# Kernel optimization log

Measured on AMD Instinct MI355X. Metric: run time of the kernel, lower is better.

The kernel has to match this reference:

```python
import jax, jax.numpy as jnp
import numpy as np

DEPTH = 7  # complete binary trees with 2**DEPTH = 128 leaves

B, L = 4096, 128
V, E, OUT = 100000, 128, 3


def setup_inputs() -> dict:
    key = jax.random.key(0)
    ks = jax.random.split(key, 6)
    tokens = jax.random.randint(ks[0], (B, L), 0, V, dtype=jnp.int64)
    embedding = jax.random.normal(ks[1], (V, E), dtype=jnp.float32)
    # tree_layer: Linear(2E -> E); torch stores weight as [out, in]
    W_tree = jax.random.normal(ks[2], (E, 2 * E), dtype=jnp.float32) * (1.0 / np.sqrt(2 * E))
    b_tree = jax.random.normal(ks[3], (E,), dtype=jnp.float32) * 0.01
    # classifier_layer: Linear(E -> OUT)
    W_cls = jax.random.normal(ks[4], (OUT, E), dtype=jnp.float32) * (1.0 / np.sqrt(E))
    b_cls = jax.random.normal(ks[5], (OUT,), dtype=jnp.float32) * 0.01
    return {"tokens": tokens, "embedding": embedding, "W_tree": W_tree,
            "b_tree": b_tree, "W_cls": W_cls, "b_cls": b_cls}


def reference(tokens, embedding, W_tree, b_tree, W_cls, b_cls):
    # Leaf embeddings: gather rows of the embedding table. [B, L, E]
    reps = embedding[tokens]
    # Level-synchronous bottom-up composition (depth-batched across all trees):
    # at each level, pair adjacent nodes, concat features, apply tree_layer + tanh.
    for _ in range(DEPTH):
        left = reps[:, 0::2, :]   # [B, n/2, E]
        right = reps[:, 1::2, :]  # [B, n/2, E]
        combined = jnp.concatenate([left, right], axis=-1)  # [B, n/2, 2E]
        reps = jnp.tanh(jnp.einsum('bnh,eh->bne', combined, W_tree) + b_tree)
    roots = reps[:, 0, :]  # [B, E]
    return roots @ W_cls.T + b_cls  # [B, OUT]
```

## Files before the change

### kernel.cpp

```cpp
#include <hip/hip_runtime.h>
#include <hip/hip_fp16.h>


typedef _Float16 half8 __attribute__((ext_vector_type(8)));
typedef float floatx4 __attribute__((ext_vector_type(4)));

#define STRIDE 264
#define UROW   33
#define NPAIR  2048

__device__ __forceinline__ float fast_tanh(float x) {
  float e = __expf(2.f * x);
  return 1.f - 2.f * __builtin_amdgcn_rcpf(e + 1.f);
}

__device__ __forceinline__ unsigned pkrtz(float a, float b) {
  auto h = __builtin_amdgcn_cvt_pkrtz(a, b);
  return __builtin_bit_cast(unsigned, h);
}

__device__ __forceinline__ void gather_leafhalf(int tok, const float* __restrict__ emb,
                                                _Float16* buf, int row, int seg) {
  const float4* src = (const float4*)emb + (size_t)tok * 32 + (seg & 1) * 16;
  uint4* dst = (uint4*)buf + row * UROW + seg * 8;
#pragma unroll
  for (int j = 0; j < 8; ++j) {
    float4 x = src[2 * j], y = src[2 * j + 1];
    uint4 w;
    w.x = pkrtz(x.x, x.y); w.y = pkrtz(x.z, x.w);
    w.z = pkrtz(y.x, y.y); w.w = pkrtz(y.z, y.w);
    dst[j] = w;
  }
}

__device__ __forceinline__ void mfma_k256(const _Float16* arow, const half8 (&Wf)[2][8],
                                          floatx4 (&accO)[2]) {
  floatx4 aA[2], aB[2];
  aA[0] = (floatx4){0.f, 0.f, 0.f, 0.f}; aA[1] = (floatx4){0.f, 0.f, 0.f, 0.f};
  aB[0] = (floatx4){0.f, 0.f, 0.f, 0.f}; aB[1] = (floatx4){0.f, 0.f, 0.f, 0.f};
#pragma unroll
  for (int ks = 0; ks < 4; ++ks) {
    half8 x0 = *(const half8*)(arow + ks * 32);
    half8 x1 = *(const half8*)(arow + (ks + 4) * 32);
    aA[0] = __builtin_amdgcn_mfma_f32_16x16x32_f16(x0, Wf[0][ks],     aA[0], 0, 0, 0);
    aB[0] = __builtin_amdgcn_mfma_f32_16x16x32_f16(x1, Wf[0][ks + 4], aB[0], 0, 0, 0);
    aA[1] = __builtin_amdgcn_mfma_f32_16x16x32_f16(x0, Wf[1][ks],     aA[1], 0, 0, 0);
    aB[1] = __builtin_amdgcn_mfma_f32_16x16x32_f16(x1, Wf[1][ks + 4], aB[1], 0, 0, 0);
  }
  accO[0] = aA[0] + aB[0];
  accO[1] = aA[1] + aB[1];
}

template<int MT, int MOUT>
__device__ __forceinline__ void level_std(
    const _Float16* inb, _Float16* outb,
    const half8 (&Wf)[2][8], const float (&bias)[2],
    int nbase, int l15, int quad)
{
  floatx4 acc[MT][2];
  if (MT == 1) {
    floatx4 a2[2];
    mfma_k256(inb + l15 * STRIDE + quad * 8, Wf, a2);
    acc[0][0] = a2[0]; acc[0][1] = a2[1];
  } else {
#pragma unroll
    for (int m = 0; m < MT; ++m) {
      acc[m][0] = (floatx4){0.f, 0.f, 0.f, 0.f};
      acc[m][1] = (floatx4){0.f, 0.f, 0.f, 0.f};
    }
#pragma unroll
    for (int m = 0; m < MT; ++m) {
      const _Float16* arow = inb + (m * 16 + l15) * STRIDE + quad * 8;
#pragma unroll
      for (int ks = 0; ks < 8; ++ks) {
        half8 a = *(const half8*)(arow + ks * 32);
        acc[m][0] = __builtin_amdgcn_mfma_f32_16x16x32_f16(a, Wf[0][ks], acc[m][0], 0, 0, 0);
        acc[m][1] = __builtin_amdgcn_mfma_f32_16x16x32_f16(a, Wf[1][ks], acc[m][1], 0, 0, 0);
      }
    }
  }

  const int mrow = quad * 4;
#pragma unroll
  for (int m = 0; m < MT; ++m)
#pragma unroll
    for (int i = 0; i < 2; ++i) {
      const int col = (nbase + i) * 16 + l15;
#pragma unroll
      for (int r = 0; r < 4; ++r) {
        const int node = m * 16 + mrow + r;
        if (node < MOUT) {
          float v = fast_tanh(acc[m][i][r] + bias[i]);
          outb[(node >> 1) * STRIDE + (node & 1) * 128 + col] = (_Float16)v;
        }
      }
    }
}

__global__ __launch_bounds__(256, 3)
void tree_kernel(const int* __restrict__ tokens,
                 const float* __restrict__ embedding,
                 const float* __restrict__ W_tree,
                 const float* __restrict__ b_tree,
                 const float* __restrict__ W_cls,
                 const float* __restrict__ b_cls,
                 float* __restrict__ out)
{
  __shared__ __align__(16) _Float16 bufA[64 * STRIDE];
  __shared__ __align__(16) _Float16 bufB[32 * STRIDE];
  __shared__ __align__(16) _Float16 bufC[4 * STRIDE];
  __shared__ float wavepart[4][2][3];

  const int tid  = threadIdx.x;
  const int wid  = tid >> 6;
  const int lane = tid & 63;
  const int l15  = lane & 15;
  const int quad = lane >> 4;
  const int nbase = wid * 2;
  const int row  = tid & 63;
  const int seg  = tid >> 6;
  const int tidx = 2 * row + (seg >> 1);

  half8 Wf[2][8];
#pragma unroll
  for (int i = 0; i < 2; ++i) {
    const int e = (nbase + i) * 16 + l15;
#pragma unroll
    for (int ks = 0; ks < 8; ++ks) {
      const int k = ks * 32 + quad * 8;
      const float4* p = (const float4*)(W_tree + e * 256 + k);
      float4 lo = p[0], hi = p[1];
      half8 f;
      f[0] = (_Float16)lo.x; f[1] = (_Float16)lo.y; f[2] = (_Float16)lo.z; f[3] = (_Float16)lo.w;
      f[4] = (_Float16)hi.x; f[5] = (_Float16)hi.y; f[6] = (_Float16)hi.z; f[7] = (_Float16)hi.w;
      Wf[i][ks] = f;
    }
  }
  float bias[2];
#pragma unroll
  for (int i = 0; i < 2; ++i) bias[i] = b_tree[(nbase + i) * 16 + l15];

  float wc[2][3];
#pragma unroll
  for (int i = 0; i < 2; ++i) {
    const int col = (nbase + i) * 16 + l15;
#pragma unroll
    for (int o = 0; o < 3; ++o) wc[i][o] = W_cls[o * 128 + col];
  }

  int tokA = tokens[(2 * blockIdx.x) * 128 + tidx];

#pragma unroll 1
  for (int p = blockIdx.x; p < NPAIR; p += gridDim.x) {
    int pn = p + gridDim.x;
    if (pn >= NPAIR) pn = p;

    gather_leafhalf(tokA, embedding, bufA, row, seg);
    const int tokB = tokens[(2 * p + 1) * 128 + tidx];
    __syncthreads();

    level_std<4, 64>(bufA, bufB, Wf, bias, nbase, l15, quad);
    __syncthreads();
    level_std<2, 32>(bufB, bufA, Wf, bias, nbase, l15, quad);
    __syncthreads();
    level_std<1, 16>(bufA, bufB, Wf, bias, nbase, l15, quad);
    __syncthreads();
    level_std<1,  8>(bufB, bufA, Wf, bias, nbase, l15, quad);
    __syncthreads();
    level_std<1,  4>(bufA, bufC, Wf, bias, nbase, l15, quad);
    __syncthreads();

    gather_leafhalf(tokB, embedding, bufA, row, seg);
    tokA = tokens[(2 * pn) * 128 + tidx];
    __syncthreads();

    level_std<4, 64>(bufA, bufB, Wf, bias, nbase, l15, quad);
    __syncthreads();
    level_std<2, 32>(bufB, bufA, Wf, bias, nbase, l15, quad);
    __syncthreads();
    level_std<1, 16>(bufA, bufB, Wf, bias, nbase, l15, quad);
    __syncthreads();
    level_std<1,  8>(bufB, bufA, Wf, bias, nbase, l15, quad);
    __syncthreads();
    level_std<1,  4>(bufA, bufC + 2 * STRIDE, Wf, bias, nbase, l15, quad);
    __syncthreads();

    {
      const int rclamp = l15 < 4 ? l15 : 3;
      floatx4 acc[2];
      mfma_k256(bufC + rclamp * STRIDE + quad * 8, Wf, acc);
      const int mrow = quad * 4;
#pragma unroll
      for (int i = 0; i < 2; ++i) {
        const int col = (nbase + i) * 16 + l15;
#pragma unroll
        for (int r = 0; r < 4; ++r) {
          const int mr = mrow + r;
          if (mr < 4) {
            float v = fast_tanh(acc[i][r] + bias[i]);
            bufA[(mr >> 1) * STRIDE + (mr & 1) * 128 + col] = (_Float16)v;
          }
        }
      }
    }
    __syncthreads();

    {
      floatx4 acc[2];
      mfma_k256(bufA + l15 * STRIDE + quad * 8, Wf, acc);
      float part[2][3] = {{0.f, 0.f, 0.f}, {0.f, 0.f, 0.f}};
      if (quad == 0) {
#pragma unroll
        for (int i = 0; i < 2; ++i) {
#pragma unroll
          for (int rr = 0; rr < 2; ++rr) {
            float v = fast_tanh(acc[i][rr] + bias[i]);
#pragma unroll
            for (int o = 0; o < 3; ++o) part[rr][o] = fmaf(v, wc[i][o], part[rr][o]);
          }
        }
      }
#pragma unroll
      for (int rr = 0; rr < 2; ++rr) {
#pragma unroll
        for (int o = 0; o < 3; ++o) {
          float v = part[rr][o];
          v += __shfl_down(v, 8);
          v += __shfl_down(v, 4);
          v += __shfl_down(v, 2);
          v += __shfl_down(v, 1);
          if (lane == 0) wavepart[wid][rr][o] = v;
        }
      }
    }
    __syncthreads();
    if (tid < 6) {
      const int rr = tid / 3, o = tid - 3 * rr;
      float v = wavepart[0][rr][o] + wavepart[1][rr][o]
              + wavepart[2][rr][o] + wavepart[3][rr][o];
      out[(2 * p + rr) * 3 + o] = v + b_cls[o];
    }
  }
}

extern "C" void kernel_launch(void* const* d_in, const int* in_sizes, int n_in,
                              void* d_out, int out_size, void* d_ws, size_t ws_size,
                              hipStream_t stream) {
  const int*   tokens    = (const int*)d_in[0];
  const float* embedding = (const float*)d_in[1];
  const float* W_tree    = (const float*)d_in[2];
  const float* b_tree    = (const float*)d_in[3];
  const float* W_cls     = (const float*)d_in[4];
  const float* b_cls     = (const float*)d_in[5];
  float* out = (float*)d_out;

  dim3 grid(768), block(256);
  tree_kernel<<<grid, block, 0, stream>>>(tokens, embedding, W_tree, b_tree, W_cls, b_cls, out);
}
```

Measured before the change: 155.6 us.

## Split waves across M and N halves with 4-column weight tiles per wave

Each wave now holds weights for four 16-column output tiles (half of N) instead of two, and the M dimension is split between wave pairs, so each A fragment loaded from LDS feeds four MFMAs. The deep levels have each wave handle only two of its four column tiles. Launch bounds drop to one block per SIMD group and the grid shrinks from 768 to 512 blocks to match the doubled weight-register footprint. This trades occupancy and latency hiding for fewer LDS reads per MFMA.

```diff
diff --git a/kernel.cpp b/kernel.cpp
--- a/kernel.cpp
+++ b/kernel.cpp
@@ -33,8 +33,50 @@
   }
 }
 
-__device__ __forceinline__ void mfma_k256(const _Float16* arow, const half8 (&Wf)[2][8],
-                                          floatx4 (&accO)[2]) {
+template<int MTW, int MOUT>
+__device__ __forceinline__ void level_m(
+    const _Float16* inb, _Float16* outb,
+    const half8 (&Wf)[4][8], const float (&bias)[4],
+    int m0, int nbase, int l15, int quad)
+{
+#pragma unroll
+  for (int m = 0; m < MTW; ++m) {
+    const int gm = m0 + m;
+    const _Float16* arow = inb + (gm * 16 + l15) * STRIDE + quad * 8;
+    floatx4 acc[4];
+#pragma unroll
+    for (int i = 0; i < 4; ++i) acc[i] = (floatx4){0.f, 0.f, 0.f, 0.f};
+#pragma unroll
+    for (int ks = 0; ks < 8; ++ks) {
+      half8 a = *(const half8*)(arow + ks * 32);
+#pragma unroll
+      for (int i = 0; i < 4; ++i)
+        acc[i] = __builtin_amdgcn_mfma_f32_16x16x32_f16(a, Wf[i][ks], acc[i], 0, 0, 0);
+    }
+    const int mrow = quad * 4;
+#pragma unroll
+    for (int i = 0; i < 4; ++i) {
+      const int col = (nbase + i) * 16 + l15;
+#pragma unroll
+      for (int r = 0; r < 4; ++r) {
+        const int node = gm * 16 + mrow + r;
+        if (node < MOUT) {
+          float v = fast_tanh(acc[i][r] + bias[i]);
+          outb[(node >> 1) * STRIDE + (node & 1) * 128 + col] = (_Float16)v;
+        }
+      }
+    }
+  }
+}
+
+template<int MOUT, int RCLAMP>
+__device__ __forceinline__ void level_deep(
+    const _Float16* inb, _Float16* outb,
+    const half8 (&Wf)[4][8], const float (&bias)[4],
+    int d0, int nbase, int l15, int quad)
+{
+  const int rr = l15 < RCLAMP ? l15 : RCLAMP;
+  const _Float16* arow = inb + rr * STRIDE + quad * 8;
   floatx4 aA[2], aB[2];
   aA[0] = (floatx4){0.f, 0.f, 0.f, 0.f}; aA[1] = (floatx4){0.f, 0.f, 0.f, 0.f};
   aB[0] = (floatx4){0.f, 0.f, 0.f, 0.f}; aB[1] = (floatx4){0.f, 0.f, 0.f, 0.f};
@@ -42,62 +84,29 @@
   for (int ks = 0; ks < 4; ++ks) {
     half8 x0 = *(const half8*)(arow + ks * 32);
     half8 x1 = *(const half8*)(arow + (ks + 4) * 32);
-    aA[0] = __builtin_amdgcn_mfma_f32_16x16x32_f16(x0, Wf[0][ks],     aA[0], 0, 0, 0);
-    aB[0] = __builtin_amdgcn_mfma_f32_16x16x32_f16(x1, Wf[0][ks + 4], aB[0], 0, 0, 0);
-    aA[1] = __builtin_amdgcn_mfma_f32_16x16x32_f16(x0, Wf[1][ks],     aA[1], 0, 0, 0);
-    aB[1] = __builtin_amdgcn_mfma_f32_16x16x32_f16(x1, Wf[1][ks + 4], aB[1], 0, 0, 0);
-  }
-  accO[0] = aA[0] + aB[0];
-  accO[1] = aA[1] + aB[1];
-}
-
-template<int MT, int MOUT>
-__device__ __forceinline__ void level_std(
-    const _Float16* inb, _Float16* outb,
-    const half8 (&Wf)[2][8], const float (&bias)[2],
-    int nbase, int l15, int quad)
-{
-  floatx4 acc[MT][2];
-  if (MT == 1) {
-    floatx4 a2[2];
-    mfma_k256(inb + l15 * STRIDE + quad * 8, Wf, a2);
-    acc[0][0] = a2[0]; acc[0][1] = a2[1];
-  } else {
-#pragma unroll
-    for (int m = 0; m < MT; ++m) {
-      acc[m][0] = (floatx4){0.f, 0.f, 0.f, 0.f};
-      acc[m][1] = (floatx4){0.f, 0.f, 0.f, 0.f};
-    }
-#pragma unroll
-    for (int m = 0; m < MT; ++m) {
-      const _Float16* arow = inb + (m * 16 + l15) * STRIDE + quad * 8;
-#pragma unroll
-      for (int ks = 0; ks < 8; ++ks) {
-        half8 a = *(const half8*)(arow + ks * 32);
-        acc[m][0] = __builtin_amdgcn_mfma_f32_16x16x32_f16(a, Wf[0][ks], acc[m][0], 0, 0, 0);
-        acc[m][1] = __builtin_amdgcn_mfma_f32_16x16x32_f16(a, Wf[1][ks], acc[m][1], 0, 0, 0);
-      }
-    }
-  }
-
+    aA[0] = __builtin_amdgcn_mfma_f32_16x16x32_f16(x0, Wf[d0][ks],         aA[0], 0, 0, 0);
+    aB[0] = __builtin_amdgcn_mfma_f32_16x16x32_f16(x1, Wf[d0][ks + 4],     aB[0], 0, 0, 0);
+    aA[1] = __builtin_amdgcn_mfma_f32_16x16x32_f16(x0, Wf[d0 + 1][ks],     aA[1], 0, 0, 0);
+    aB[1] = __builtin_amdgcn_mfma_f32_16x16x32_f16(x1, Wf[d0 + 1][ks + 4], aB[1], 0, 0, 0);
+  }
   const int mrow = quad * 4;
 #pragma unroll
-  for (int m = 0; m < MT; ++m)
-#pragma unroll
-    for (int i = 0; i < 2; ++i) {
-      const int col = (nbase + i) * 16 + l15;
-#pragma unroll
-      for (int r = 0; r < 4; ++r) {
-        const int node = m * 16 + mrow + r;
-        if (node < MOUT) {
-          float v = fast_tanh(acc[m][i][r] + bias[i]);
-          outb[(node >> 1) * STRIDE + (node & 1) * 128 + col] = (_Float16)v;
-        }
-      }
-    }
-}
-
-__global__ __launch_bounds__(256, 3)
+  for (int i = 0; i < 2; ++i) {
+    floatx4 acc = aA[i] + aB[i];
+    const int col = (nbase + d0 + i) * 16 + l15;
+    const float b = bias[d0 + i];
+#pragma unroll
+    for (int r = 0; r < 4; ++r) {
+      const int node = mrow + r;
+      if (node < MOUT) {
+        float v = fast_tanh(acc[r] + b);
+        outb[(node >> 1) * STRIDE + (node & 1) * 128 + col] = (_Float16)v;
+      }
+    }
+  }
+}
+
+__global__ __launch_bounds__(256, 1)
 void tree_kernel(const int* __restrict__ tokens,
                  const float* __restrict__ embedding,
                  const float* __restrict__ W_tree,
@@ -116,14 +125,16 @@
   const int lane = tid & 63;
   const int l15  = lane & 15;
   const int quad = lane >> 4;
-  const int nbase = wid * 2;
+  const int nbase = (wid & 1) * 4;
+  const int mhalf = wid >> 1;
+  const int d0    = mhalf * 2;
   const int row  = tid & 63;
   const int seg  = tid >> 6;
   const int tidx = 2 * row + (seg >> 1);
 
-  half8 Wf[2][8];
-#pragma unroll
-  for (int i = 0; i < 2; ++i) {
+  half8 Wf[4][8];
+#pragma unroll
+  for (int i = 0; i < 4; ++i) {
     const int e = (nbase + i) * 16 + l15;
 #pragma unroll
     for (int ks = 0; ks < 8; ++ks) {
@@ -136,13 +147,13 @@
       Wf[i][ks] = f;
     }
   }
-  float bias[2];
-#pragma unroll
-  for (int i = 0; i < 2; ++i) bias[i] = b_tree[(nbase + i) * 16 + l15];
-
-  float wc[2][3];
-#pragma unroll
-  for (int i = 0; i < 2; ++i) {
+  float bias[4];
+#pragma unroll
+  for (int i = 0; i < 4; ++i) bias[i] = b_tree[(nbase + i) * 16 + l15];
+
+  float wc[4][3];
+#pragma unroll
+  for (int i = 0; i < 4; ++i) {
     const int col = (nbase + i) * 16 + l15;
 #pragma unroll
     for (int o = 0; o < 3; ++o) wc[i][o] = W_cls[o * 128 + col];
@@ -158,87 +169,81 @@
     gather_leafhalf(tokA, embedding, bufA, row, seg);
     const int tokB = tokens[(2 * p + 1) * 128 + tidx];
     __syncthreads();
-
-    level_std<4, 64>(bufA, bufB, Wf, bias, nbase, l15, quad);
-    __syncthreads();
-    level_std<2, 32>(bufB, bufA, Wf, bias, nbase, l15, quad);
-    __syncthreads();
-    level_std<1, 16>(bufA, bufB, Wf, bias, nbase, l15, quad);
-    __syncthreads();
-    level_std<1,  8>(bufB, bufA, Wf, bias, nbase, l15, quad);
-    __syncthreads();
-    level_std<1,  4>(bufA, bufC, Wf, bias, nbase, l15, quad);
+    level_m<2, 64>(bufA, bufB, Wf, bias, mhalf * 2, nbase, l15, quad);
+    __syncthreads();
+    level_m<1, 32>(bufB, bufA, Wf, bias, mhalf,     nbase, l15, quad);
+    __syncthreads();
+    level_deep<16, 15>(bufA, bufB, Wf, bias, d0, nbase, l15, quad);
+    __syncthreads();
+    level_deep< 8,  7>(bufB, bufA, Wf, bias, d0, nbase, l15, quad);
+    __syncthreads();
+    level_deep< 4,  3>(bufA, bufC, Wf, bias, d0, nbase, l15, quad);
     __syncthreads();
 
     gather_leafhalf(tokB, embedding, bufA, row, seg);
     tokA = tokens[(2 * pn) * 128 + tidx];
     __syncthreads();
-
-    level_std<4, 64>(bufA, bufB, Wf, bias, nbase, l15, quad);
-    __syncthreads();
-    level_std<2, 32>(bufB, bufA, Wf, bias, nbase, l15, quad);
-    __syncthreads();
-    level_std<1, 16>(bufA, bufB, Wf, bias, nbase, l15, quad);
-    __syncthreads();
-    level_std<1,  8>(bufB, bufA, Wf, bias, nbase, l15, quad);
-    __syncthreads();
-    level_std<1,  4>(bufA, bufC + 2 * STRIDE, Wf, bias, nbase, l15, quad);
+    level_m<2, 64>(bufA, bufB, Wf, bias, mhalf * 2, nbase, l15, quad);
+    __syncthreads();
+    level_m<1, 32>(bufB, bufA, Wf, bias, mhalf,     nbase, l15, quad);
+    __syncthreads();
+    level_deep<16, 15>(bufA, bufB, Wf, bias, d0, nbase, l15, quad);
+    __syncthreads();
+    level_deep< 8,  7>(bufB, bufA, Wf, bias, d0, nbase, l15, quad);
+    __syncthreads();
+    level_deep< 4,  3>(bufA, bufC + 2 * STRIDE, Wf, bias, d0, nbase, l15, quad);
+    __syncthreads();
+
+    level_deep<4, 3>(bufC, bufA, Wf, bias, d0, nbase, l15, quad);
     __syncthreads();
 
     {
-      const int rclamp = l15 < 4 ? l15 : 3;
-      floatx4 acc[2];
-      mfma_k256(bufC + rclamp * STRIDE + quad * 8, Wf, acc);
-      const int mrow = quad * 4;
-#pragma unroll
-      for (int i = 0; i < 2; ++i) {
-        const int col = (nbase + i) * 16 + l15;
-#pragma unroll
-        for (int r = 0; r < 4; ++r) {
-          const int mr = mrow + r;
-          if (mr < 4) {
-            float v = fast_tanh(acc[i][r] + bias[i]);
-            bufA[(mr >> 1) * STRIDE + (mr & 1) * 128 + col] = (_Float16)v;
+      const int rr = l15 < 1 ? l15 : 1;
+      const _Float16* arow = bufA + rr * STRIDE + quad * 8;
+      floatx4 aA[2], aB[2];
+      aA[0] = (floatx4){0.f, 0.f, 0.f, 0.f}; aA[1] = (floatx4){0.f, 0.f, 0.f, 0.f};
+      aB[0] = (floatx4){0.f, 0.f, 0.f, 0.f}; aB[1] = (floatx4){0.f, 0.f, 0.f, 0.f};
+#pragma unroll
+      for (int ks = 0; ks < 4; ++ks) {
+        half8 x0 = *(const half8*)(arow + ks * 32);
+        half8 x1 = *(const half8*)(arow + (ks + 4) * 32);
+        aA[0] = __builtin_amdgcn_mfma_f32_16x16x32_f16(x0, Wf[d0][ks],         aA[0], 0, 0, 0);
+        aB[0] = __builtin_amdgcn_mfma_f32_16x16x32_f16(x1, Wf[d0][ks + 4],     aB[0], 0, 0, 0);
+        aA[1] = __builtin_amdgcn_mfma_f32_16x16x32_f16(x0, Wf[d0 + 1][ks],     aA[1], 0, 0, 0);
+        aB[1] = __builtin_amdgcn_mfma_f32_16x16x32_f16(x1, Wf[d0 + 1][ks + 4], aB[1], 0, 0, 0);
+      }
+      float part[2][3] = {{0.f, 0.f, 0.f}, {0.f, 0.f, 0.f}};
+      if (quad == 0) {
+#pragma unroll
+        for (int i = 0; i < 2; ++i) {
+          floatx4 acc = aA[i] + aB[i];
+#pragma unroll
+          for (int s = 0; s < 2; ++s) {
+            float v = fast_tanh(acc[s] + bias[d0 + i]);
+#pragma unroll
+            for (int o = 0; o < 3; ++o) part[s][o] = fmaf(v, wc[d0 + i][o], part[s][o]);
           }
         }
       }
-    }
-    __syncthreads();
-
-    {
-      floatx4 acc[2];
-      mfma_k256(bufA + l15 * STRIDE + quad * 8, Wf, acc);
-      float part[2][3] = {{0.f, 0.f, 0.f}, {0.f, 0.f, 0.f}};
-      if (quad == 0) {
-#pragma unroll
-        for (int i = 0; i < 2; ++i) {
-#pragma unroll
-          for (int rr = 0; rr < 2; ++rr) {
-            float v = fast_tanh(acc[i][rr] + bias[i]);
-#pragma unroll
-            for (int o = 0; o < 3; ++o) part[rr][o] = fmaf(v, wc[i][o], part[rr][o]);
-          }
-        }
-      }
-#pragma unroll
-      for (int rr = 0; rr < 2; ++rr) {
+#pragma unroll
+      for (int s = 0; s < 2; ++s) {
 #pragma unroll
         for (int o = 0; o < 3; ++o) {
-          float v = part[rr][o];
+          float v = part[s][o];
           v += __shfl_down(v, 8);
           v += __shfl_down(v, 4);
           v += __shfl_down(v, 2);
           v += __shfl_down(v, 1);
-          if (lane == 0) wavepart[wid][rr][o] = v;
+          if (lane == 0) wavepart[wid][s][o] = v;
         }
       }
     }
     __syncthreads();
     if (tid < 6) {
-      const int rr = tid / 3, o = tid - 3 * rr;
-      float v = wavepart[0][rr][o] + wavepart[1][rr][o]
-              + wavepart[2][rr][o] + wavepart[3][rr][o];
-      out[(2 * p + rr) * 3 + o] = v + b_cls[o];
+      const int s = tid / 3, o = tid - 3 * s;
+      float v = wavepart[0][s][o] + wavepart[1][s][o]
+              + wavepart[2][s][o] + wavepart[3][s][o];
+      out[(2 * p + s) * 3 + o] = v + b_cls[o];
     }
   }
 }
@@ -254,6 +259,6 @@
   const float* b_cls     = (const float*)d_in[5];
   float* out = (float*)d_out;
 
-  dim3 grid(768), block(256);
+  dim3 grid(512), block(256);
   tree_kernel<<<grid, block, 0, stream>>>(tokens, embedding, W_tree, b_tree, W_cls, b_cls, out);
 }
```

After: 290.6 us. 86.8% more time.
